# Kernel tuning notes

Hardware: AMD Instinct MI355X
Metric: run time of the kernel (lower is better)

The kernel has to match this reference:

```python
import jax, jax.numpy as jnp
import numpy as np

N, E = 40000, 640000
D, H, DK = 128, 8, 16   # out_dim, n_heads, d_k = D // H
T, R = 3, 4             # num node types, num relation types


def setup_inputs() -> dict:
    key = jax.random.key(0)
    ks = jax.random.split(key, 16)
    glorot = lambda k, shape, fan: jax.random.normal(k, shape, jnp.float32) * np.sqrt(2.0 / fan)
    inp = {
        'node_inp': jax.random.normal(ks[0], (N, D), jnp.float32),
        'node_type': jax.random.randint(ks[1], (N,), 0, T),
        'edge_index': jax.random.randint(ks[2], (2, E), 0, N),
        'edge_type': jax.random.randint(ks[3], (E,), 0, R),
        'node_position': jax.random.randint(ks[4], (N,), 0, N),
        # per-node-type Linear weights, stored [T, in, out] (y = x @ W + b)
        'Kw': glorot(ks[5], (T, D, D), 2 * D), 'Kb': jnp.zeros((T, D), jnp.float32),
        'Qw': glorot(ks[6], (T, D, D), 2 * D), 'Qb': jnp.zeros((T, D), jnp.float32),
        'Vw': glorot(ks[7], (T, D, D), 2 * D), 'Vb': jnp.zeros((T, D), jnp.float32),
        'Aw': glorot(ks[8], (T, D, D), 2 * D), 'Ab': jnp.zeros((T, D), jnp.float32),
        'relation_pri': jnp.ones((T, R, T, H), jnp.float32),
        'relation_att': glorot(ks[9], (R, H, DK, DK), 2 * DK),
        'relation_msg': glorot(ks[10], (R, H, DK, DK), 2 * DK),
        'relation_s2u': glorot(ks[11], (D, D), 2 * D),
        'skip': jnp.ones((T,), jnp.float32),
    }
    return inp


def reference(node_inp, node_type, edge_index, edge_type, node_position,
              Kw, Kb, Qw, Qb, Vw, Vb, Aw, Ab,
              relation_pri, relation_att, relation_msg, relation_s2u, skip):
    n = node_inp.shape[0]
    src, tgt = edge_index[0], edge_index[1]  # j (source), i (target)
    ar = jnp.arange(n)

    # per-type K/Q/V projections for every node: [T, N, D], then select own type
    k_all = jnp.einsum('nd,tdo->tno', node_inp, Kw) + Kb[:, None, :]
    q_all = jnp.einsum('nd,tdo->tno', node_inp, Qw) + Qb[:, None, :]
    v_all = jnp.einsum('nd,tdo->tno', node_inp, Vw) + Vb[:, None, :]
    k_node = k_all[node_type, ar]
    q_node = q_all[node_type, ar]
    v_node = v_all[node_type, ar]

    k_j = k_node[src].reshape(-1, H, DK)
    v_j = v_node[src].reshape(-1, H, DK)
    q_i = q_node[tgt].reshape(-1, H, DK)

    # per-relation attention / message transforms (select per edge relation)
    k_t = jnp.zeros_like(k_j)
    v_t = jnp.zeros_like(v_j)
    for r in range(R):
        sel = (edge_type == r)[:, None, None]
        k_t = jnp.where(sel, jnp.einsum('ehd,hdf->ehf', k_j, relation_att[r]), k_t)
        v_t = jnp.where(sel, jnp.einsum('ehd,hdf->ehf', v_j, relation_msg[r]), v_t)

    st, tt = node_type[src], node_type[tgt]
    pri = relation_pri[tt, edge_type, st]                       # [E, H]
    att_raw = (q_i * k_t).sum(-1) * pri / np.sqrt(DK)           # [E, H]

    # scatter-softmax over edges sharing the same target node
    m = jax.ops.segment_max(att_raw, tgt, num_segments=n)
    m = jnp.where(jnp.isfinite(m), m, 0.0)
    ex = jnp.exp(att_raw - m[tgt])
    den = jax.ops.segment_sum(ex, tgt, num_segments=n)
    att = ex / (den[tgt] + 1e-16)

    msg = (v_t * att[:, :, None]).reshape(-1, D)
    aggr = jax.ops.segment_sum(msg, tgt, num_segments=n)        # scatter-add

    # speaker information: edges with edge_type==0, message from target rep to source index
    sp_in = v_all[1][tgt]                                       # v_linears[1](node_inp[edge_index_i])
    sp_msg = sp_in @ relation_s2u                               # [E, D]
    drop_idx = jnp.where(edge_type == 0, src, n)                # out-of-range -> dropped
    speaker_info = jnp.zeros((n, D), node_inp.dtype).at[drop_idx].set(sp_msg, mode='drop')

    aggr = jax.nn.gelu(aggr + speaker_info, approximate=False)

    # target-specific aggregation with per-type learnable skip (dropout=eval identity)
    a_all = jnp.einsum('no,tof->tnf', aggr, Aw) + Ab[:, None, :]
    a_node = a_all[node_type, ar]
    alpha = jax.nn.sigmoid(skip)[node_type][:, None]
    return a_node * alpha + node_inp * (1.0 - alpha)
```

## Files before the change

kernel.cpp:

```cpp
#include <hip/hip_runtime.h>
#include <hip/hip_bf16.h>
#include <math.h>

#define ND 128
#define NH 8
#define DKK 16
#define NT 3
#define NR 4
#define NB 8
#define NMAT 12
#define SCB 4096

typedef unsigned short ushort_t;
typedef __bf16 bf16_t;
typedef bf16_t bf16x8 __attribute__((ext_vector_type(8)));
typedef float f32x4 __attribute__((ext_vector_type(4)));

__device__ __forceinline__ float bf2f(unsigned short u) {
    union { unsigned int i; float f; } v; v.i = ((unsigned int)u) << 16; return v.f;
}
__device__ __forceinline__ unsigned short f2bf(float f) {
    union { float f; unsigned int i; } v; v.f = f;
    unsigned int x = v.i;
    unsigned int lsb = (x >> 16) & 1u;
    x += 0x7fffu + lsb;
    return (unsigned short)(x >> 16);
}
__device__ __forceinline__ unsigned int pk2(float a, float b) {
    return (unsigned int)f2bf(a) | ((unsigned int)f2bf(b) << 16);
}
__device__ __forceinline__ void load_bf8(const ushort_t* p, float* o) {
    uint4 u = *reinterpret_cast<const uint4*>(p);
    o[0]=bf2f(u.x & 0xffff); o[1]=bf2f(u.x >> 16);
    o[2]=bf2f(u.y & 0xffff); o[3]=bf2f(u.y >> 16);
    o[4]=bf2f(u.z & 0xffff); o[5]=bf2f(u.z >> 16);
    o[6]=bf2f(u.w & 0xffff); o[7]=bf2f(u.w >> 16);
}
__device__ __forceinline__ bf16x8 as_bf16x8(uint4 u) {
    union { uint4 u; bf16x8 v; } c; c.u = u; return c.v;
}


__global__ void k_zero(int n, int* offs, int* winner, int* tcnt) {
    int i = blockIdx.x * 256 + threadIdx.x;
    if (i < n) { offs[i] = 0; winner[i] = -1; }
    if (i < NT) tcnt[i] = 0;
}

__global__ void k_count(int n, int e, const int* src, const int* tgt, const int* etype,
                        const int* ntype, int* offs, int* winner, int* tcnt, int* rank) {
    int i = blockIdx.x * 256 + threadIdx.x;
    if (i < e) {
        rank[i] = atomicAdd(&offs[tgt[i]], 1);
        if (etype[i] == 0) atomicMax(&winner[src[i]], i);
    }
    if (i < n) {
        int t = ntype[i];
        int lane = threadIdx.x & 63;
        #pragma unroll
        for (int tt = 0; tt < NT; tt++) {
            bool me = (t == tt);
            unsigned long long m = __ballot(me);
            if (me) {
                int lower = __popcll(m & ((1ull << lane) - 1ull));
                if (lower == 0) atomicAdd(&tcnt[tt], __popcll(m));
            }
        }
    }
}


__global__ void k_scanA(int n, const int* offs, int* bsum) {
    __shared__ int red[256];
    int b = blockIdx.x, tid = threadIdx.x;
    int base = b * SCB + tid * 16;
    int s = 0;
    #pragma unroll
    for (int i = 0; i < 16; i++) {
        int idx = base + i;
        if (idx < n) s += offs[idx];
    }
    red[tid] = s;
    __syncthreads();
    for (int d = 128; d > 0; d >>= 1) {
        if (tid < d) red[tid] += red[tid + d];
        __syncthreads();
    }
    if (tid == 0) bsum[b] = red[0];
}

__global__ void k_scanB(int nb, const int* bsum, int* boff,
                        const int* tcnt, int* tnext, int* tstart) {
    if (threadIdx.x == 0) {
        int run = 0;
        for (int b = 0; b < nb; b++) { boff[b] = run; run += bsum[b]; }
        int t0 = 0;
        for (int t = 0; t < NT; t++) { tnext[t] = t0; tstart[t] = t0; t0 += tcnt[t]; }
    }
}

__global__ void k_scanC(int n, int* offs, const int* boff) {
    __shared__ int red[256];
    int b = blockIdx.x, tid = threadIdx.x;
    int base = b * SCB + tid * 16;
    int v[16];
    int s = 0;
    #pragma unroll
    for (int i = 0; i < 16; i++) {
        int idx = base + i;
        v[i] = (idx < n) ? offs[idx] : 0;
        s += v[i];
    }
    red[tid] = s;
    __syncthreads();
    for (int d = 1; d < 256; d <<= 1) {
        int vv = (tid >= d) ? red[tid - d] : 0;
        __syncthreads();
        red[tid] += vv;
        __syncthreads();
    }
    int run = boff[b] + red[tid] - s;
    #pragma unroll
    for (int i = 0; i < 16; i++) {
        int idx = base + i;
        if (idx < n) { offs[idx] = run; run += v[i]; }
    }
    if (base <= n && n < base + 16) offs[n] = run;
}

__global__ void k_scatter(int n, int e, const int* src, const int* tgt, const int* etype,
                          const int* ntype, const int* offs, const int* rank,
                          int* eord, int mode, int* tnext, int* order) {
    int i = blockIdx.x * 256 + threadIdx.x;
    if (i < e) {
        int p = offs[tgt[i]] + rank[i];
        if (mode) {
            int s = src[i];
            eord[p] = (s * NR + etype[i]) | (ntype[s] << 28);
        } else {
            eord[p] = i;
        }
    }
    if (i < n) {
        int t = ntype[i];
        int lane = threadIdx.x & 63;
        #pragma unroll
        for (int tt = 0; tt < NT; tt++) {
            bool me = (t == tt);
            unsigned long long m = __ballot(me);
            if (me) {
                int lower = __popcll(m & ((1ull << lane) - 1ull));
                int leader = __ffsll((long long)m) - 1;
                int base = 0;
                if (lane == leader) base = atomicAdd(&tnext[tt], __popcll(m));
                base = __shfl(base, leader, 64);
                order[base + lower] = i;
            }
        }
    }
}


__global__ void k_pack(const float* Qw, const float* Qb, const float* Kw, const float* Kb,
                       const float* Vw, const float* Vb, const float* Aw, const float* Ab,
                       const float* s2u, const float* r_att, const float* r_msg,
                       ushort_t* Wall, float* bcat) {
    int blk = blockIdx.x;
    int kb = blk & 3;
    int c = (blk >> 2) & 7;
    int tm = blk >> 5;
    int m = tm % NMAT, t = tm / NMAT;
    int lane = threadIdx.x;
    int nn = c * 16 + (lane & 15);
    int quad = lane >> 4;
    int k0 = kb * 32 + quad * 8;
    ushort_t* dst = Wall + (size_t)blk * 512 + lane * 8;

    if (m == 0 || m == 5 || m == 10 || m == 11) {
        const float* W; const float* B;
        if (m == 0)       { W = Qw + (size_t)t * ND * ND; B = Qb + t * ND; }
        else if (m == 5)  { W = Vw + (size_t)ND * ND;     B = Vb + ND; }
        else if (m == 10) { W = Aw + (size_t)t * ND * ND; B = Ab + t * ND; }
        else              { W = s2u;                      B = nullptr; }
        #pragma unroll
        for (int j = 0; j < 8; j++) dst[j] = f2bf(W[(size_t)(k0 + j) * ND + nn]);
        if (kb == 0 && quad == 0)
            bcat[(t * NMAT + m) * ND + nn] = B ? B[nn] : 0.f;
    } else {
        int r = (m <= 4) ? (m - 1) : (m - 6);
        const float* W0 = (m <= 4) ? Kw : Vw;
        const float* B0 = (m <= 4) ? Kb : Vb;
        const float* Wr = (m <= 4) ? r_att : r_msg;
        int h = c, f = lane & 15;
        float wcol[16];
        #pragma unroll
        for (int jj = 0; jj < 16; jj++)
            wcol[jj] = Wr[(((size_t)r * NH + h) * DKK + jj) * DKK + f];
        #pragma unroll
        for (int j = 0; j < 8; j++) {
            const float* row = W0 + ((size_t)t * ND + (k0 + j)) * ND + h * DKK;
            float s = 0.f;
            #pragma unroll
            for (int jj = 0; jj < 16; jj++) s += row[jj] * wcol[jj];
            dst[j] = f2bf(s);
        }
        if (kb == 0 && quad == 0) {
            const float* brow = B0 + t * ND + h * DKK;
            float sb = 0.f;
            #pragma unroll
            for (int jj = 0; jj < 16; jj++) sb += brow[jj] * wcol[jj];
            bcat[(t * NMAT + m) * ND + nn] = sb;
        }
    }
}

__global__ void __launch_bounds__(256) k_projm(
    int n, const float* x_in, const int* order,
    const int* tcnt, const int* tstart,
    const ushort_t* Wall, const float* bcat,
    int m0, int nm,
    ushort_t* out_qn, ushort_t* out_kt, ushort_t* out_v1, ushort_t* out_vt)
{
    __shared__ __align__(16) ushort_t xs[4096];
    __shared__ int nodes[32];
    int b = blockIdx.x;
    int nb0 = (tcnt[0] + 31) >> 5, nb1 = (tcnt[1] + 31) >> 5, nb2 = (tcnt[2] + 31) >> 5;
    int t, lb;
    if (b < nb0)                  { t = 0; lb = b; }
    else if (b < nb0 + nb1)       { t = 1; lb = b - nb0; }
    else if (b < nb0 + nb1 + nb2) { t = 2; lb = b - nb0 - nb1; }
    else return;
    int segoff = lb * 32;
    int cnt = min(32, tcnt[t] - segoff);
    int segbase = tstart[t] + segoff;
    int tid = threadIdx.x;
    if (tid < 32) nodes[tid] = (tid < cnt) ? order[segbase + tid] : -1;
    __syncthreads();
    {
        int row = tid >> 3;
        int d0 = (tid & 7) * 16;
        int rt = row >> 4, rl = row & 15;
        int kb = d0 >> 5, q0 = (d0 >> 3) & 3;
        uint4 c0, c1;
        if (row < cnt) {
            const float4* xp4 = (const float4*)(x_in + (size_t)nodes[row] * ND + d0);
            float4 a = xp4[0], b2 = xp4[1], c2 = xp4[2], d4 = xp4[3];
            c0.x = pk2(a.x, a.y);   c0.y = pk2(a.z, a.w);
            c0.z = pk2(b2.x, b2.y); c0.w = pk2(b2.z, b2.w);
            c1.x = pk2(c2.x, c2.y); c1.y = pk2(c2.z, c2.w);
            c1.z = pk2(d4.x, d4.y); c1.w = pk2(d4.z, d4.w);
        } else {
            c0.x = c0.y = c0.z = c0.w = 0u;
            c1 = c0;
        }
        *(uint4*)&xs[((rt * 4 + kb) * 64 + q0 * 16 + rl) * 8]       = c0;
        *(uint4*)&xs[((rt * 4 + kb) * 64 + (q0 + 1) * 16 + rl) * 8] = c1;
    }
    __syncthreads();

    int w = tid >> 6, lane = tid & 63;
    int rt = w & 1;
    bf16x8 afr[4];
    #pragma unroll
    for (int kb = 0; kb < 4; kb++)
        afr[kb] = as_bf16x8(*(const uint4*)&xs[((rt * 4 + kb) * 64 + lane) * 8]);
    int nct = nm * 8;
    for (int ct = (w >> 1); ct < nct; ct += 2) {
        int m = m0 + (ct >> 3), c = ct & 7;
        const uint4* bp = (const uint4*)(Wall + ((((size_t)t * NMAT + m) * 8 + c) * 4) * 512);
        f32x4 acc = {0.f, 0.f, 0.f, 0.f};
        #pragma unroll
        for (int kb = 0; kb < 4; kb++) {
            bf16x8 bfr = as_bf16x8(bp[kb * 64 + lane]);
            acc = __builtin_amdgcn_mfma_f32_16x16x32_bf16(afr[kb], bfr, acc, 0, 0, 0);
        }
        int col = c * 16 + (lane & 15);
        float bias = bcat[(t * NMAT + m) * ND + col];
        int rbase = rt * 16 + (lane >> 4) * 4;
        #pragma unroll
        for (int r = 0; r < 4; r++) {
            int grow = rbase + r;
            if (grow >= cnt) continue;
            int node = nodes[grow];
            ushort_t val = f2bf(acc[r] + bias);
            if (m == 0)       out_qn[(size_t)node * ND + col] = val;
            else if (m <= 4)  out_kt[((size_t)node * NR + (m - 1)) * ND + col] = val;
            else if (m == 5)  out_v1[(size_t)node * ND + col] = val;
            else              out_vt[((size_t)node * NR + (m - 6)) * ND + col] = val;
        }
    }
}

__global__ void __launch_bounds__(256) k_projall(
    int n, const float* x_in, const int* order,
    const int* tcnt, const int* tstart,
    const ushort_t* Wall, const float* bcat,
    ushort_t* out_qn, ushort_t* out_kt, ushort_t* out_v1, ushort_t* out_vt)
{
    __shared__ __align__(16) ushort_t xs[4096];
    __shared__ int nodes[32];
    int b = blockIdx.x;
    int nb0 = (tcnt[0] + 31) >> 5, nb1 = (tcnt[1] + 31) >> 5, nb2 = (tcnt[2] + 31) >> 5;
    int t, lb;
    if (b < nb0)                  { t = 0; lb = b; }
    else if (b < nb0 + nb1)       { t = 1; lb = b - nb0; }
    else if (b < nb0 + nb1 + nb2) { t = 2; lb = b - nb0 - nb1; }
    else return;
    int segoff = lb * 32;
    int cnt = min(32, tcnt[t] - segoff);
    int segbase = tstart[t] + segoff;
    int tid = threadIdx.x;
    if (tid < 32) nodes[tid] = (tid < cnt) ? order[segbase + tid] : -1;
    __syncthreads();
    {
        int row = tid >> 3;
        int d0 = (tid & 7) * 16;
        int rt = row >> 4, rl = row & 15;
        int kb = d0 >> 5, q0 = (d0 >> 3) & 3;
        uint4 c0, c1;
        if (row < cnt) {
            const float4* xp4 = (const float4*)(x_in + (size_t)nodes[row] * ND + d0);
            float4 a = xp4[0], b2 = xp4[1], c2 = xp4[2], d4 = xp4[3];
            c0.x = pk2(a.x, a.y);   c0.y = pk2(a.z, a.w);
            c0.z = pk2(b2.x, b2.y); c0.w = pk2(b2.z, b2.w);
            c1.x = pk2(c2.x, c2.y); c1.y = pk2(c2.z, c2.w);
            c1.z = pk2(d4.x, d4.y); c1.w = pk2(d4.z, d4.w);
        } else {
            c0.x = c0.y = c0.z = c0.w = 0u;
            c1 = c0;
        }
        *(uint4*)&xs[((rt * 4 + kb) * 64 + q0 * 16 + rl) * 8]       = c0;
        *(uint4*)&xs[((rt * 4 + kb) * 64 + (q0 + 1) * 16 + rl) * 8] = c1;
    }
    __syncthreads();

    int w = tid >> 6, lane = tid & 63;
    int rt = w & 1;
    bf16x8 afr[4];
    #pragma unroll
    for (int kb = 0; kb < 4; kb++)
        afr[kb] = as_bf16x8(*(const uint4*)&xs[((rt * 4 + kb) * 64 + lane) * 8]);
    for (int ct = (w >> 1); ct < 80; ct += 2) {
        int m = ct >> 3, c = ct & 7;
        const uint4* bp = (const uint4*)(Wall + ((((size_t)t * NMAT + m) * 8 + c) * 4) * 512);
        f32x4 acc = {0.f, 0.f, 0.f, 0.f};
        #pragma unroll
        for (int kb = 0; kb < 4; kb++) {
            bf16x8 bfr = as_bf16x8(bp[kb * 64 + lane]);
            acc = __builtin_amdgcn_mfma_f32_16x16x32_bf16(afr[kb], bfr, acc, 0, 0, 0);
        }
        int col = c * 16 + (lane & 15);
        float bias = bcat[(t * NMAT + m) * ND + col];
        int rbase = rt * 16 + (lane >> 4) * 4;
        #pragma unroll
        for (int r = 0; r < 4; r++) {
            int grow = rbase + r;
            if (grow >= cnt) continue;
            int node = nodes[grow];
            ushort_t val = f2bf(acc[r] + bias);
            if (m == 0)       out_qn[(size_t)node * ND + col] = val;
            else if (m <= 4)  out_kt[((size_t)node * NR + (m - 1)) * ND + col] = val;
            else if (m == 5)  out_v1[(size_t)node * ND + col] = val;
            else              out_vt[((size_t)node * NR + (m - 6)) * ND + col] = val;
        }
    }
}

__global__ void __launch_bounds__(256) k_flash(
    int n, const int* off, const int* srp, const int* ntype,
    const ushort_t* qn, const ushort_t* kt, const ushort_t* vt,
    const float* r_pri, float* aggr)
{
    int wv = threadIdx.x >> 6, lane = threadIdx.x & 63;
    int i = blockIdx.x * 4 + wv;
    if (i >= n) return;
    int h = lane & 7, slot = lane >> 3;
    int hA = lane >> 3;
    int tt = ntype[i];
    float qf[16];
    load_bf8(qn + (size_t)i * ND + h * DKK, qf);
    load_bf8(qn + (size_t)i * ND + h * DKK + 8, qf + 8);
    const float* prib = r_pri + (size_t)(tt * NR * NT) * NH + h;
    int d0 = off[i], d1 = off[i + 1];
    float m = -3.0e38f, den = 0.f;
    float acc0 = 0.f, acc1 = 0.f;
    for (int p0 = d0; p0 < d1; p0 += 8) {
        int p = p0 + slot;
        bool live = (p < d1);
        int sp = live ? srp[p] : 0;
        int sr = sp & 0x0fffffff;
        int st = ((unsigned int)sp) >> 28;
        int r = sr & (NR - 1);
        float kf[16];
        const ushort_t* kp = kt + (size_t)sr * ND + h * DKK;
        load_bf8(kp, kf);
        load_bf8(kp + 8, kf + 8);
        float a = 0.f;
        #pragma unroll
        for (int f = 0; f < 16; f++) a += qf[f] * kf[f];
        float pri = prib[(r * NT + st) * NH];
        float logit = fminf(fmaxf(a * pri * 0.25f, -1.0e4f), 1.0e4f);
        if (!live) logit = -3.0e38f;
        float cm = logit;
        #pragma unroll
        for (int d = 8; d < 64; d <<= 1) cm = fmaxf(cm, __shfl_xor(cm, d, 64));
        float mnew = fmaxf(m, cm);
        float w = live ? expf(logit - mnew) : 0.f;
        float ws = w;
        #pragma unroll
        for (int d = 8; d < 64; d <<= 1) ws += __shfl_xor(ws, d, 64);
        float scale = expf(m - mnew);
        den = den * scale + ws;
        m = mnew;
        float scaleA = __shfl(scale, hA, 64);
        acc0 *= scaleA; acc1 *= scaleA;
        #pragma unroll
        for (int s = 0; s < 8; s++) {
            if (p0 + s < d1) {
                int srcl = s * 8 + hA;
                int srb  = __shfl(sr, srcl, 64);
                float wb = __shfl(w, srcl, 64);
                unsigned int u = *reinterpret_cast<const unsigned int*>(
                    vt + (size_t)srb * ND + lane * 2);
                acc0 += wb * bf2f(u & 0xffff);
                acc1 += wb * bf2f(u >> 16);
            }
        }
    }
    float denA = __shfl(den, hA, 64);
    float inv = 1.f / (denA + 1e-16f);
    float2 o; o.x = acc0 * inv; o.y = acc1 * inv;
    *reinterpret_cast<float2*>(aggr + (size_t)i * ND + lane * 2) = o;
}

__global__ void __launch_bounds__(256) k_sfinal(
    int n, const float* x_in, const int* order, const int* tcnt, const int* tstart,
    const int* winner, const int* tgt, const ushort_t* v1b,
    const ushort_t* Wall, const float* bcat, const float* skip,
    const float* aggr, float* out)
{
    __shared__ __align__(16) float xf[32 * 132];
    __shared__ __align__(16) ushort_t xs[4096];
    __shared__ int nodes[32];
    __shared__ int wsrc[32];
    int b = blockIdx.x;
    int nb0 = (tcnt[0] + 31) >> 5, nb1 = (tcnt[1] + 31) >> 5, nb2 = (tcnt[2] + 31) >> 5;
    int t, lb;
    if (b < nb0)                  { t = 0; lb = b; }
    else if (b < nb0 + nb1)       { t = 1; lb = b - nb0; }
    else if (b < nb0 + nb1 + nb2) { t = 2; lb = b - nb0 - nb1; }
    else return;
    int segoff = lb * 32;
    int cnt = min(32, tcnt[t] - segoff);
    int segbase = tstart[t] + segoff;
    int tid = threadIdx.x;
    if (tid < 32) {
        int nd = (tid < cnt) ? order[segbase + tid] : -1;
        nodes[tid] = nd;
        int wi = (nd >= 0) ? winner[nd] : -1;
        wsrc[tid] = (wi >= 0) ? tgt[wi] : -1;
    }
    __syncthreads();
    {
        int row = tid >> 3;
        int d0 = (tid & 7) * 16;
        int rt = row >> 4, rl = row & 15;
        int kb = d0 >> 5, q0 = (d0 >> 3) & 3;
        uint4 c0, c1;
        int s = (row < cnt) ? wsrc[row] : -1;
        if (s >= 0) {
            const uint4* vp = (const uint4*)(v1b + (size_t)s * ND + d0);
            c0 = vp[0]; c1 = vp[1];
        } else { c0.x = c0.y = c0.z = c0.w = 0u; c1 = c0; }
        *(uint4*)&xs[((rt * 4 + kb) * 64 + q0 * 16 + rl) * 8]       = c0;
        *(uint4*)&xs[((rt * 4 + kb) * 64 + (q0 + 1) * 16 + rl) * 8] = c1;
    }
    __syncthreads();
    int w = tid >> 6, lane = tid & 63;
    int rt = w & 1;
    {
        bf16x8 afr[4];
        #pragma unroll
        for (int kb = 0; kb < 4; kb++)
            afr[kb] = as_bf16x8(*(const uint4*)&xs[((rt * 4 + kb) * 64 + lane) * 8]);
        for (int ct = (w >> 1); ct < 8; ct += 2) {
            const uint4* bp = (const uint4*)(Wall + (((size_t)11 * 8 + ct) * 4) * 512);
            f32x4 acc = {0.f, 0.f, 0.f, 0.f};
            #pragma unroll
            for (int kb = 0; kb < 4; kb++) {
                bf16x8 bfr = as_bf16x8(bp[kb * 64 + lane]);
                acc = __builtin_amdgcn_mfma_f32_16x16x32_bf16(afr[kb], bfr, acc, 0, 0, 0);
            }
            int col = ct * 16 + (lane & 15);
            int rbase = rt * 16 + (lane >> 4) * 4;
            #pragma unroll
            for (int r = 0; r < 4; r++) {
                int grow = rbase + r;
                if (grow >= cnt) continue;
                int node = nodes[grow];
                float g = aggr[(size_t)node * ND + col] + acc[r];
                g = 0.5f * g * (1.f + erff(g * 0.70710678118f));
                xf[grow * 132 + col] = g;
            }
        }
    }
    __syncthreads();
    {
        int row = tid >> 3;
        int d0 = (tid & 7) * 16;
        int rt2 = row >> 4, rl = row & 15;
        int kb = d0 >> 5, q0 = (d0 >> 3) & 3;
        uint4 c0, c1;
        if (row < cnt) {
            const float4* xp4 = (const float4*)(xf + row * 132 + d0);
            float4 a = xp4[0], b2 = xp4[1], c2 = xp4[2], d4 = xp4[3];
            c0.x = pk2(a.x, a.y);   c0.y = pk2(a.z, a.w);
            c0.z = pk2(b2.x, b2.y); c0.w = pk2(b2.z, b2.w);
            c1.x = pk2(c2.x, c2.y); c1.y = pk2(c2.z, c2.w);
            c1.z = pk2(d4.x, d4.y); c1.w = pk2(d4.z, d4.w);
        } else {
            c0.x = c0.y = c0.z = c0.w = 0u;
            c1 = c0;
        }
        *(uint4*)&xs[((rt2 * 4 + kb) * 64 + q0 * 16 + rl) * 8]       = c0;
        *(uint4*)&xs[((rt2 * 4 + kb) * 64 + (q0 + 1) * 16 + rl) * 8] = c1;
    }
    __syncthreads();
    float alpha = 1.f / (1.f + expf(-skip[t]));
    {
        bf16x8 afr[4];
        #pragma unroll
        for (int kb = 0; kb < 4; kb++)
            afr[kb] = as_bf16x8(*(const uint4*)&xs[((rt * 4 + kb) * 64 + lane) * 8]);
        for (int ct = (w >> 1); ct < 8; ct += 2) {
            const uint4* bp = (const uint4*)(Wall + ((((size_t)t * NMAT + 10) * 8 + ct) * 4) * 512);
            f32x4 acc = {0.f, 0.f, 0.f, 0.f};
            #pragma unroll
            for (int kb = 0; kb < 4; kb++) {
                bf16x8 bfr = as_bf16x8(bp[kb * 64 + lane]);
                acc = __builtin_amdgcn_mfma_f32_16x16x32_bf16(afr[kb], bfr, acc, 0, 0, 0);
            }
            int col = ct * 16 + (lane & 15);
            float bias = bcat[(t * NMAT + 10) * ND + col];
            int rbase = rt * 16 + (lane >> 4) * 4;
            #pragma unroll
            for (int r = 0; r < 4; r++) {
                int grow = rbase + r;
                if (grow >= cnt) continue;
                int node = nodes[grow];
                float xin = x_in[(size_t)node * ND + col];
                out[(size_t)node * ND + col] = (acc[r] + bias) * alpha + xin * (1.f - alpha);
            }
        }
    }
}

__global__ void __launch_bounds__(256) k_attmd(
    int n, const int* off, const int* srp, const int* ntype,
    const ushort_t* qn, const ushort_t* kt, const float* r_pri,
    float* atts, ushort_t* mb, float* db)
{
    int wv = threadIdx.x >> 6, lane = threadIdx.x & 63;
    int i = blockIdx.x * 4 + wv;
    if (i >= n) return;
    int h = lane & 7, slot = lane >> 3;
    int tt = ntype[i];
    float qf[16];
    load_bf8(qn + (size_t)i * ND + h * DKK, qf);
    load_bf8(qn + (size_t)i * ND + h * DKK + 8, qf + 8);
    const float* prib = r_pri + (size_t)(tt * NR * NT) * NH + h;
    int d0 = off[i], d1 = off[i + 1];
    float m = -3.0e38f, den = 0.f;
    #pragma unroll 2
    for (int p0 = d0; p0 < d1; p0 += 8) {
        int p = p0 + slot;
        bool live = (p < d1);
        int sp = live ? srp[p] : 0;
        int sr = sp & 0x0fffffff;
        int st = ((unsigned int)sp) >> 28;
        int r = sr & (NR - 1);
        float kf[16];
        const ushort_t* kp = kt + (size_t)sr * ND + h * DKK;
        load_bf8(kp, kf);
        load_bf8(kp + 8, kf + 8);
        float a = 0.f;
        #pragma unroll
        for (int f = 0; f < 16; f++) a += qf[f] * kf[f];
        float pri = prib[(r * NT + st) * NH];
        float logit = fminf(fmaxf(a * pri * 0.25f, -1.0e4f), 1.0e4f);
        if (live) {
            atts[(size_t)p * NH + h] = logit;
            float mnew = fmaxf(m, logit);
            den = den * expf(m - mnew) + expf(logit - mnew);
            m = mnew;
        }
    }
    #pragma unroll
    for (int d = 8; d < 64; d <<= 1) {
        float mo = __shfl_xor(m, d, 64);
        float dn = __shfl_xor(den, d, 64);
        float mnew = fmaxf(m, mo);
        den = den * expf(m - mnew) + dn * expf(mo - mnew);
        m = mnew;
    }
    if (slot == 0) {
        ushort_t mh = (d1 > d0) ? f2bf(m) : (ushort_t)0;
        float dfin = (d1 > d0) ? den * expf(m - bf2f(mh)) : 0.f;
        mb[i * NH + h] = mh;
        db[i * NH + h] = dfin;
    }
}

__global__ void __launch_bounds__(256) k_aggr_fast(
    int n, const int* off, const int* srp, const ushort_t* vt, const float* atts,
    const ushort_t* mb, const float* db, float* aggr)
{
    int wv = threadIdx.x >> 6, lane = threadIdx.x & 63;
    int i = blockIdx.x * 4 + wv;
    if (i >= n) return;
    int h = lane >> 3;
    float mref = bf2f(mb[i * NH + h]);
    float inv = 1.f / (db[i * NH + h] + 1e-16f);
    int d0 = off[i], d1 = off[i + 1];
    float acc0 = 0.f, acc1 = 0.f;
    #pragma unroll 4
    for (int p = d0; p < d1; p++) {
        int sr = srp[p] & 0x0fffffff;
        float w = expf(atts[(size_t)p * NH + h] - mref) * inv;
        unsigned int u = *reinterpret_cast<const unsigned int*>(
            vt + (size_t)sr * ND + lane * 2);
        acc0 += w * bf2f(u & 0xffff);
        acc1 += w * bf2f(u >> 16);
    }
    float2 o; o.x = acc0; o.y = acc1;
    *reinterpret_cast<float2*>(aggr + (size_t)i * ND + lane * 2) = o;
}


__global__ void k_proj(int n, const float* x_in, const int* ntype, const int* order,
                       const float* Kw, const float* Kb,
                       const float* Qw, const float* Qb,
                       const float* Vw, const float* Vb,
                       ushort_t* kn, ushort_t* qn, ushort_t* vn, ushort_t* v1) {
    __shared__ float xs[NB][ND];
    __shared__ int nodes[NB];
    __shared__ int types[NB];
    int tid = threadIdx.x;
    int base = blockIdx.x * NB;
    int cnt = min(NB, n - base);
    if (tid < cnt) { int nd = order[base + tid]; nodes[tid] = nd; types[tid] = ntype[nd]; }
    __syncthreads();
    for (int j = 0; j < cnt; j++) xs[j][tid] = x_in[(size_t)nodes[j] * ND + tid];
    __syncthreads();
    bool uni = (types[0] == types[cnt - 1]);
    for (int m = 0; m < 4; m++) {
        const float *W, *B; ushort_t* out; int forced_t = -1;
        if (m == 0)      { W = Kw; B = Kb; out = kn; }
        else if (m == 1) { W = Qw; B = Qb; out = qn; }
        else if (m == 2) { W = Vw; B = Vb; out = vn; }
        else             { W = Vw; B = Vb; out = v1; forced_t = 1; }
        if (uni || forced_t >= 0) {
            int t = (forced_t >= 0) ? forced_t : types[0];
            float bias = B[t * ND + tid];
            float acc[NB];
            #pragma unroll
            for (int j = 0; j < NB; j++) acc[j] = bias;
            const float* Wp = W + (size_t)t * ND * ND + tid;
            for (int d = 0; d < ND; d++) {
                float w = Wp[(size_t)d * ND];
                #pragma unroll
                for (int j = 0; j < NB; j++) acc[j] += xs[j][d] * w;
            }
            for (int j = 0; j < cnt; j++) out[(size_t)nodes[j] * ND + tid] = f2bf(acc[j]);
        } else {
            for (int j = 0; j < cnt; j++) {
                int t = types[j];
                float acc = B[t * ND + tid];
                const float* Wp = W + (size_t)t * ND * ND + tid;
                for (int d = 0; d < ND; d++) acc += xs[j][d] * Wp[(size_t)d * ND];
                out[(size_t)nodes[j] * ND + tid] = f2bf(acc);
            }
        }
    }
}

__global__ void k_att(int e, const int* src, const int* tgt, const int* etype, const int* ntype,
                      const ushort_t* kn, const ushort_t* qn,
                      const float* r_att, const float* r_pri, float* att) {
    int id = blockIdx.x * 256 + threadIdx.x;
    if (id >= e * NH) return;
    int ee = id >> 3, h = id & 7;
    int s = src[ee], t = tgt[ee], r = etype[ee];
    float kf[16], qf[16];
    load_bf8(kn + (size_t)s * ND + h * DKK, kf);
    load_bf8(kn + (size_t)s * ND + h * DKK + 8, kf + 8);
    load_bf8(qn + (size_t)t * ND + h * DKK, qf);
    load_bf8(qn + (size_t)t * ND + h * DKK + 8, qf + 8);
    const float* W = r_att + (size_t)(r * NH + h) * DKK * DKK;
    float kt[16];
    #pragma unroll
    for (int f = 0; f < 16; f++) kt[f] = 0.f;
    #pragma unroll 4
    for (int d = 0; d < 16; d++) {
        float kd = kf[d];
        #pragma unroll
        for (int f = 0; f < 16; f++) kt[f] += kd * W[d * 16 + f];
    }
    float a = 0.f;
    #pragma unroll
    for (int f = 0; f < 16; f++) a += qf[f] * kt[f];
    int tt = ntype[t], st = ntype[s];
    float pri = r_pri[((tt * NR + r) * NT + st) * NH + h];
    float logit = a * pri * 0.25f;
    logit = fminf(fmaxf(logit, -1.0e4f), 1.0e4f);
    att[(size_t)ee * NH + h] = logit;
}

__global__ void k_mden(int n, const int* off, const int* sorted,
                       const float* att, ushort_t* mb, float* db) {
    int id = blockIdx.x * 256 + threadIdx.x;
    if (id >= n * NH) return;
    int i = id >> 3, h = id & 7;
    int d0 = off[i], d1 = off[i + 1];
    float m = -3.0e38f;
    for (int p = d0; p < d1; p++) m = fmaxf(m, att[(size_t)sorted[p] * NH + h]);
    ushort_t mh = (d1 > d0) ? f2bf(m) : (ushort_t)0;
    float mref = bf2f(mh);
    float den = 0.f;
    for (int p = d0; p < d1; p++) den += expf(att[(size_t)sorted[p] * NH + h] - mref);
    mb[id] = mh;
    db[id] = den;
}

__global__ void k_norm(int e, const int* tgt, const ushort_t* mb, const float* db, float* att) {
    int id = blockIdx.x * 256 + threadIdx.x;
    if (id >= e * NH) return;
    int ee = id >> 3, h = id & 7;
    int t = tgt[ee];
    float w = expf(att[id] - bf2f(mb[t * NH + h])) / (db[t * NH + h] + 1e-16f);
    att[id] = w;
}

__global__ void k_aggr(int n, const int* off, const int* sorted, const int* src, const int* etype,
                       const ushort_t* vn, const float* r_msg, const float* att, float* aggr) {
    int wv = threadIdx.x >> 6, lane = threadIdx.x & 63;
    int i = blockIdx.x * 4 + wv;
    if (i >= n) return;
    int h = lane >> 3, f0 = (lane & 7) * 2;
    int d0 = off[i], d1 = off[i + 1];
    float acc0 = 0.f, acc1 = 0.f;
    for (int p = d0; p < d1; p++) {
        int ee = sorted[p];
        int s = src[ee], r = etype[ee];
        float w = att[(size_t)ee * NH + h];
        float vj[16];
        load_bf8(vn + (size_t)s * ND + h * DKK, vj);
        load_bf8(vn + (size_t)s * ND + h * DKK + 8, vj + 8);
        const float* Wm = r_msg + (size_t)(r * NH + h) * DKK * DKK + f0;
        float a0 = 0.f, a1 = 0.f;
        #pragma unroll
        for (int d = 0; d < 16; d++) {
            a0 += vj[d] * Wm[d * 16];
            a1 += vj[d] * Wm[d * 16 + 1];
        }
        acc0 += w * a0; acc1 += w * a1;
    }
    aggr[(size_t)i * ND + h * DKK + f0]     = acc0;
    aggr[(size_t)i * ND + h * DKK + f0 + 1] = acc1;
}

__global__ void k_spk(int n, const int* winner, const int* tgt, const ushort_t* v1,
                      const float* s2u, float* aggr) {
    __shared__ float xs[NB][ND];
    __shared__ int wn[NB];
    int tid = threadIdx.x;
    int base = blockIdx.x * NB;
    int cnt = min(NB, n - base);
    if (tid < cnt) wn[tid] = winner[base + tid];
    __syncthreads();
    for (int j = 0; j < cnt; j++) {
        int w = wn[j];
        xs[j][tid] = (w >= 0) ? bf2f(v1[(size_t)tgt[w] * ND + tid]) : 0.f;
    }
    __syncthreads();
    float acc[NB];
    #pragma unroll
    for (int j = 0; j < NB; j++) acc[j] = 0.f;
    const float* Wp = s2u + tid;
    for (int d = 0; d < ND; d++) {
        float w = Wp[(size_t)d * ND];
        #pragma unroll
        for (int j = 0; j < NB; j++) acc[j] += xs[j][d] * w;
    }
    for (int j = 0; j < cnt; j++) {
        size_t idx = (size_t)(base + j) * ND + tid;
        float g = aggr[idx] + acc[j];
        g = 0.5f * g * (1.f + erff(g * 0.70710678118f));
        aggr[idx] = g;
    }
}

__global__ void k_final(int n, const float* x_in, const int* ntype, const int* order,
                        const float* Aw, const float* Ab, const float* skip,
                        const float* aggr, float* out) {
    __shared__ float xs[NB][ND];
    __shared__ int nodes[NB];
    __shared__ int types[NB];
    int tid = threadIdx.x;
    int base = blockIdx.x * NB;
    int cnt = min(NB, n - base);
    if (tid < cnt) { int nd = order[base + tid]; nodes[tid] = nd; types[tid] = ntype[nd]; }
    __syncthreads();
    for (int j = 0; j < cnt; j++) xs[j][tid] = aggr[(size_t)nodes[j] * ND + tid];
    __syncthreads();
    bool uni = (types[0] == types[cnt - 1]);
    if (uni) {
        int t = types[0];
        float bias = Ab[t * ND + tid];
        float acc[NB];
        #pragma unroll
        for (int j = 0; j < NB; j++) acc[j] = bias;
        const float* Wp = Aw + (size_t)t * ND * ND + tid;
        for (int d = 0; d < ND; d++) {
            float w = Wp[(size_t)d * ND];
            #pragma unroll
            for (int j = 0; j < NB; j++) acc[j] += xs[j][d] * w;
        }
        float alpha = 1.f / (1.f + expf(-skip[t]));
        for (int j = 0; j < cnt; j++) {
            float xin = x_in[(size_t)nodes[j] * ND + tid];
            out[(size_t)nodes[j] * ND + tid] = acc[j] * alpha + xin * (1.f - alpha);
        }
    } else {
        for (int j = 0; j < cnt; j++) {
            int t = types[j];
            float acc = Ab[t * ND + tid];
            const float* Wp = Aw + (size_t)t * ND * ND + tid;
            for (int d = 0; d < ND; d++) acc += xs[j][d] * Wp[(size_t)d * ND];
            float alpha = 1.f / (1.f + expf(-skip[t]));
            float xin = x_in[(size_t)nodes[j] * ND + tid];
            out[(size_t)nodes[j] * ND + tid] = acc * alpha + xin * (1.f - alpha);
        }
    }
}

extern "C" void kernel_launch(void* const* d_in, const int* in_sizes, int n_in,
                              void* d_out, int out_size, void* d_ws, size_t ws_size,
                              hipStream_t stream) {
    const float* node_inp = (const float*)d_in[0];
    const int* node_type  = (const int*)d_in[1];
    const int* edge_index = (const int*)d_in[2];
    const int* edge_type  = (const int*)d_in[3];
    const float* Kw = (const float*)d_in[5];
    const float* Kb = (const float*)d_in[6];
    const float* Qw = (const float*)d_in[7];
    const float* Qb = (const float*)d_in[8];
    const float* Vw = (const float*)d_in[9];
    const float* Vb = (const float*)d_in[10];
    const float* Aw = (const float*)d_in[11];
    const float* Ab = (const float*)d_in[12];
    const float* r_pri = (const float*)d_in[13];
    const float* r_att = (const float*)d_in[14];
    const float* r_msg = (const float*)d_in[15];
    const float* s2u   = (const float*)d_in[16];
    const float* skip  = (const float*)d_in[17];

    int n = in_sizes[1];
    int e = in_sizes[3];
    const int* srcp = edge_index;
    const int* tgtp = edge_index + e;

    char* wsp = (char*)d_ws;
    size_t woff = 0;
    auto alloc = [&](size_t b) { void* p = wsp + woff; woff += (b + 255) & ~(size_t)255; return p; };

    int* offs     = (int*)alloc((size_t)(n + 1) * 4);
    int* winner   = (int*)alloc((size_t)n * 4);
    int* order    = (int*)alloc((size_t)n * 4);
    int* tcnt     = (int*)alloc(16);
    int* tnext    = (int*)alloc(16);
    int* tstart   = (int*)alloc(16);
    int* bsum     = (int*)alloc(4096);
    int* boff     = (int*)alloc(4096);
    int* eord     = (int*)alloc((size_t)e * 4);
    ushort_t* mb  = (ushort_t*)alloc((size_t)n * NH * 2);
    float* db     = (float*)alloc((size_t)n * NH * 4);
    ushort_t* v1b = (ushort_t*)alloc((size_t)n * ND * 2);
    float* att    = (float*)alloc((size_t)e * NH * 4);
    size_t commonEnd = woff;

    int* rank = (int*)att;

    woff = commonEnd;
    ushort_t* WallB = (ushort_t*)alloc((size_t)NT * NMAT * 8 * 4 * 512 * 2);
    float* bcatB    = (float*)alloc((size_t)NT * NMAT * ND * 4);
    char* F         = (char*)alloc((size_t)n * 1536);
    size_t fastEnd = woff;

    woff = commonEnd;
    ushort_t* WallA = (ushort_t*)alloc((size_t)NT * NMAT * 8 * 4 * 512 * 2);
    float* bcatA    = (float*)alloc((size_t)NT * NMAT * ND * 4);
    ushort_t* qnA   = (ushort_t*)alloc((size_t)n * ND * 2);
    ushort_t* ktA   = (ushort_t*)alloc((size_t)n * NR * ND * 2);
    ushort_t* vtA   = (ushort_t*)alloc((size_t)n * NR * ND * 2);
    size_t tierAEnd = woff;
    float* aggrA = (float*)att;

    int gn = (n + 255) / 256;
    int ge = (e + 255) / 256;
    int nbscan = n / SCB + 1;
    int gproj = (n + 31) / 32 + NT;

    int tierA = (ws_size >= tierAEnd) && ((size_t)e * NH >= (size_t)n * ND);
    int fast  = (ws_size >= fastEnd);

    k_zero<<<gn, 256, 0, stream>>>(n, offs, winner, tcnt);
    k_count<<<ge, 256, 0, stream>>>(n, e, srcp, tgtp, edge_type, node_type, offs, winner, tcnt, rank);
    k_scanA<<<nbscan, 256, 0, stream>>>(n, offs, bsum);
    k_scanB<<<1, 64, 0, stream>>>(nbscan, bsum, boff, tcnt, tnext, tstart);
    k_scanC<<<nbscan, 256, 0, stream>>>(n, offs, boff);
    k_scatter<<<ge, 256, 0, stream>>>(n, e, srcp, tgtp, edge_type, node_type, offs, rank,
                                      eord, (tierA || fast) ? 1 : 0, tnext, order);

    if (tierA) {
        k_pack<<<NT * NMAT * 8 * 4, 64, 0, stream>>>(Qw, Qb, Kw, Kb, Vw, Vb, Aw, Ab,
                                                     s2u, r_att, r_msg, WallA, bcatA);
        k_projall<<<gproj, 256, 0, stream>>>(n, node_inp, order, tcnt, tstart, WallA, bcatA,
                                             qnA, ktA, v1b, vtA);
        k_flash<<<(n + 3) / 4, 256, 0, stream>>>(n, offs, eord, node_type,
                                                 qnA, ktA, vtA, r_pri, aggrA);
        k_sfinal<<<gproj, 256, 0, stream>>>(n, node_inp, order, tcnt, tstart,
                                            winner, tgtp, v1b, WallA, bcatA, skip,
                                            aggrA, (float*)d_out);
    } else if (fast) {
        ushort_t* qn  = (ushort_t*)F;
        ushort_t* kt  = (ushort_t*)(F + (size_t)n * 256);
        ushort_t* vt  = (ushort_t*)F;
        float* aggr   = (float*)(F + (size_t)n * 1024);

        k_pack<<<NT * NMAT * 8 * 4, 64, 0, stream>>>(Qw, Qb, Kw, Kb, Vw, Vb, Aw, Ab,
                                                     s2u, r_att, r_msg, WallB, bcatB);
        k_projm<<<gproj, 256, 0, stream>>>(n, node_inp, order, tcnt, tstart, WallB, bcatB,
                                           0, 6, qn, kt, v1b, (ushort_t*)nullptr);
        k_attmd<<<(n + 3) / 4, 256, 0, stream>>>(n, offs, eord, node_type,
                                                 qn, kt, r_pri, att, mb, db);
        k_projm<<<gproj, 256, 0, stream>>>(n, node_inp, order, tcnt, tstart, WallB, bcatB,
                                           6, 4, (ushort_t*)nullptr, (ushort_t*)nullptr,
                                           (ushort_t*)nullptr, vt);
        k_aggr_fast<<<(n + 3) / 4, 256, 0, stream>>>(n, offs, eord, vt, att, mb, db, aggr);
        k_sfinal<<<gproj, 256, 0, stream>>>(n, node_inp, order, tcnt, tstart,
                                            winner, tgtp, v1b, WallB, bcatB, skip,
                                            aggr, (float*)d_out);
    } else {
        woff = commonEnd;
        ushort_t* vn  = (ushort_t*)alloc((size_t)n * ND * 2);
        char* regA    = (char*)alloc((size_t)n * ND * 2 * 2);
        ushort_t* kn  = (ushort_t*)regA;
        ushort_t* qn  = (ushort_t*)(regA + (size_t)n * ND * 2);
        float* aggr   = (float*)regA;

        k_proj<<<(n + NB - 1) / NB, 128, 0, stream>>>(n, node_inp, node_type, order,
                                                      Kw, Kb, Qw, Qb, Vw, Vb, kn, qn, vn, v1b);
        k_att<<<(e * NH + 255) / 256, 256, 0, stream>>>(e, srcp, tgtp, edge_type, node_type,
                                                        kn, qn, r_att, r_pri, att);
        k_mden<<<(n * NH + 255) / 256, 256, 0, stream>>>(n, offs, eord, att, mb, db);
        k_norm<<<(e * NH + 255) / 256, 256, 0, stream>>>(e, tgtp, mb, db, att);
        k_aggr<<<(n + 3) / 4, 256, 0, stream>>>(n, offs, eord, srcp, edge_type, vn, r_msg, att, aggr);
        k_spk<<<(n + NB - 1) / NB, 128, 0, stream>>>(n, winner, tgtp, v1b, s2u, aggr);
        k_final<<<(n + NB - 1) / NB, 128, 0, stream>>>(n, node_inp, node_type, order,
                                                       Aw, Ab, skip, aggr, (float*)d_out);
    }
}
```

Baseline: 350.1 us.

## Fold relation attention into query side and apply message transform after aggregation

Instead of projecting K and V per relation for every source node (N×4 rows each), the relation attention matrix is folded into the query projection (4 per-relation queries per target), and plain K and V are stored once per node. In the flash kernel, values are accumulated into four per-relation buckets and the relation message matrix is applied once per target node after aggregation. This cuts the projection GEMM from 10 to 7 matrix slots and shrinks the per-edge gathered K/V rows from relation-expanded tables to single-row tables. In exchange it adds shared-memory query staging, extra register accumulators with branching per edge, and a per-node 16x16 shuffle-based transform at the end.

```diff
diff --git a/kernel.cpp b/kernel.cpp
--- a/kernel.cpp
+++ b/kernel.cpp
@@ -9,6 +9,7 @@
 #define NR 4
 #define NB 8
 #define NMAT 12
+#define NM2 9
 #define SCB 4096
 
 typedef unsigned short ushort_t;
@@ -210,6 +211,57 @@
             #pragma unroll
             for (int jj = 0; jj < 16; jj++) sb += brow[jj] * wcol[jj];
             bcat[(t * NMAT + m) * ND + nn] = sb;
+        }
+    }
+}
+
+__global__ void k_pack2(const float* Qw, const float* Qb, const float* Kw, const float* Kb,
+                        const float* Vw, const float* Vb, const float* Aw, const float* Ab,
+                        const float* s2u, const float* r_att,
+                        ushort_t* Wall, float* bcat) {
+    int blk = blockIdx.x;
+    int kb = blk & 3;
+    int c = (blk >> 2) & 7;
+    int tm = blk >> 5;
+    int m = tm % NM2, t = tm / NM2;
+    int lane = threadIdx.x;
+    int nn = c * 16 + (lane & 15);
+    int quad = lane >> 4;
+    int k0 = kb * 32 + quad * 8;
+    ushort_t* dst = Wall + (size_t)blk * 512 + lane * 8;
+
+    if (m >= 4) {
+        const float* W; const float* B;
+        if (m == 4)      { W = Kw + (size_t)t * ND * ND; B = Kb + t * ND; }
+        else if (m == 5) { W = Vw + (size_t)t * ND * ND; B = Vb + t * ND; }
+        else if (m == 6) { W = Vw + (size_t)ND * ND;     B = Vb + ND; }
+        else if (m == 7) { W = Aw + (size_t)t * ND * ND; B = Ab + t * ND; }
+        else             { W = s2u;                      B = nullptr; }
+        #pragma unroll
+        for (int j = 0; j < 8; j++) dst[j] = f2bf(W[(size_t)(k0 + j) * ND + nn]);
+        if (kb == 0 && quad == 0)
+            bcat[(t * NM2 + m) * ND + nn] = B ? B[nn] : 0.f;
+    } else {
+        int r = m;
+        int h = c, f = lane & 15;
+        float wrow[16];
+        #pragma unroll
+        for (int jj = 0; jj < 16; jj++)
+            wrow[jj] = r_att[(((size_t)r * NH + h) * DKK + f) * DKK + jj];
+        #pragma unroll
+        for (int j = 0; j < 8; j++) {
+            const float* row = Qw + ((size_t)t * ND + (k0 + j)) * ND + h * DKK;
+            float s = 0.f;
+            #pragma unroll
+            for (int jj = 0; jj < 16; jj++) s += row[jj] * wrow[jj];
+            dst[j] = f2bf(s);
+        }
+        if (kb == 0 && quad == 0) {
+            const float* brow = Qb + t * ND + h * DKK;
+            float sb = 0.f;
+            #pragma unroll
+            for (int jj = 0; jj < 16; jj++) sb += brow[jj] * wrow[jj];
+            bcat[(t * NM2 + m) * ND + nn] = sb;
         }
     }
 }
@@ -291,11 +343,11 @@
     }
 }
 
-__global__ void __launch_bounds__(256) k_projall(
+__global__ void __launch_bounds__(256) k_projall2(
     int n, const float* x_in, const int* order,
     const int* tcnt, const int* tstart,
     const ushort_t* Wall, const float* bcat,
-    ushort_t* out_qn, ushort_t* out_kt, ushort_t* out_v1, ushort_t* out_vt)
+    ushort_t* out_qr, ushort_t* out_kn, ushort_t* out_vn, ushort_t* out_v1)
 {
     __shared__ __align__(16) ushort_t xs[4096];
     __shared__ int nodes[32];
@@ -340,9 +392,9 @@
     #pragma unroll
     for (int kb = 0; kb < 4; kb++)
         afr[kb] = as_bf16x8(*(const uint4*)&xs[((rt * 4 + kb) * 64 + lane) * 8]);
-    for (int ct = (w >> 1); ct < 80; ct += 2) {
+    for (int ct = (w >> 1); ct < 56; ct += 2) {
         int m = ct >> 3, c = ct & 7;
-        const uint4* bp = (const uint4*)(Wall + ((((size_t)t * NMAT + m) * 8 + c) * 4) * 512);
+        const uint4* bp = (const uint4*)(Wall + ((((size_t)t * NM2 + m) * 8 + c) * 4) * 512);
         f32x4 acc = {0.f, 0.f, 0.f, 0.f};
         #pragma unroll
         for (int kb = 0; kb < 4; kb++) {
@@ -350,7 +402,7 @@
             acc = __builtin_amdgcn_mfma_f32_16x16x32_bf16(afr[kb], bfr, acc, 0, 0, 0);
         }
         int col = c * 16 + (lane & 15);
-        float bias = bcat[(t * NMAT + m) * ND + col];
+        float bias = bcat[(t * NM2 + m) * ND + col];
         int rbase = rt * 16 + (lane >> 4) * 4;
         #pragma unroll
         for (int r = 0; r < 4; r++) {
@@ -358,32 +410,37 @@
             if (grow >= cnt) continue;
             int node = nodes[grow];
             ushort_t val = f2bf(acc[r] + bias);
-            if (m == 0)       out_qn[(size_t)node * ND + col] = val;
-            else if (m <= 4)  out_kt[((size_t)node * NR + (m - 1)) * ND + col] = val;
-            else if (m == 5)  out_v1[(size_t)node * ND + col] = val;
-            else              out_vt[((size_t)node * NR + (m - 6)) * ND + col] = val;
+            if (m <= 3)       out_qr[((size_t)node * NR + m) * ND + col] = val;
+            else if (m == 4)  out_kn[(size_t)node * ND + col] = val;
+            else if (m == 5)  out_vn[(size_t)node * ND + col] = val;
+            else              out_v1[(size_t)node * ND + col] = val;
         }
     }
 }
 
 __global__ void __launch_bounds__(256) k_flash(
     int n, const int* off, const int* srp, const int* ntype,
-    const ushort_t* qn, const ushort_t* kt, const ushort_t* vt,
-    const float* r_pri, float* aggr)
+    const ushort_t* qr, const ushort_t* kn, const ushort_t* vn,
+    const float* r_pri, const float* r_msg, float* aggr)
 {
+    __shared__ float qs[4][4][132];
     int wv = threadIdx.x >> 6, lane = threadIdx.x & 63;
     int i = blockIdx.x * 4 + wv;
     if (i >= n) return;
-    int h = lane & 7, slot = lane >> 3;
-    int hA = lane >> 3;
+    {
+        int r = lane >> 4, e8 = (lane & 15) * 8;
+        float qv[8];
+        load_bf8(qr + ((size_t)i * NR + r) * ND + e8, qv);
+        #pragma unroll
+        for (int j = 0; j < 8; j++) qs[wv][r][e8 + j] = qv[j];
+    }
+    int h = lane & 7, slot = lane >> 3, hA = lane >> 3;
     int tt = ntype[i];
-    float qf[16];
-    load_bf8(qn + (size_t)i * ND + h * DKK, qf);
-    load_bf8(qn + (size_t)i * ND + h * DKK + 8, qf + 8);
     const float* prib = r_pri + (size_t)(tt * NR * NT) * NH + h;
     int d0 = off[i], d1 = off[i + 1];
     float m = -3.0e38f, den = 0.f;
-    float acc0 = 0.f, acc1 = 0.f;
+    float a00=0.f,a01=0.f,a02=0.f,a03=0.f;
+    float a10=0.f,a11=0.f,a12=0.f,a13=0.f;
     for (int p0 = d0; p0 < d1; p0 += 8) {
         int p = p0 + slot;
         bool live = (p < d1);
@@ -392,9 +449,10 @@
         int st = ((unsigned int)sp) >> 28;
         int r = sr & (NR - 1);
         float kf[16];
-        const ushort_t* kp = kt + (size_t)sr * ND + h * DKK;
+        const ushort_t* kp = kn + (size_t)(sr >> 2) * ND + h * DKK;
         load_bf8(kp, kf);
         load_bf8(kp + 8, kf + 8);
+        const float* qf = &qs[wv][r][h * DKK];
         float a = 0.f;
         #pragma unroll
         for (int f = 0; f < 16; f++) a += qf[f] * kf[f];
@@ -413,23 +471,44 @@
         den = den * scale + ws;
         m = mnew;
         float scaleA = __shfl(scale, hA, 64);
-        acc0 *= scaleA; acc1 *= scaleA;
+        a00*=scaleA; a01*=scaleA; a02*=scaleA; a03*=scaleA;
+        a10*=scaleA; a11*=scaleA; a12*=scaleA; a13*=scaleA;
         #pragma unroll
         for (int s = 0; s < 8; s++) {
             if (p0 + s < d1) {
                 int srcl = s * 8 + hA;
                 int srb  = __shfl(sr, srcl, 64);
                 float wb = __shfl(w, srcl, 64);
+                int rb = srb & 3;
                 unsigned int u = *reinterpret_cast<const unsigned int*>(
-                    vt + (size_t)srb * ND + lane * 2);
-                acc0 += wb * bf2f(u & 0xffff);
-                acc1 += wb * bf2f(u >> 16);
+                    vn + (size_t)(srb >> 2) * ND + lane * 2);
+                float v0 = wb * bf2f(u & 0xffff);
+                float v1 = wb * bf2f(u >> 16);
+                if (rb == 0)      { a00 += v0; a10 += v1; }
+                else if (rb == 1) { a01 += v0; a11 += v1; }
+                else if (rb == 2) { a02 += v0; a12 += v1; }
+                else              { a03 += v0; a13 += v1; }
             }
         }
     }
     float denA = __shfl(den, hA, 64);
     float inv = 1.f / (denA + 1e-16f);
-    float2 o; o.x = acc0 * inv; o.y = acc1 * inv;
+    int f0 = (lane & 7) * 2;
+    float o0 = 0.f, o1 = 0.f;
+    #pragma unroll
+    for (int r = 0; r < 4; r++) {
+        float ar0 = (r == 0) ? a00 : (r == 1) ? a01 : (r == 2) ? a02 : a03;
+        float ar1 = (r == 0) ? a10 : (r == 1) ? a11 : (r == 2) ? a12 : a13;
+        const float* Wm = r_msg + ((size_t)(r * NH + hA) * DKK) * DKK + f0;
+        #pragma unroll
+        for (int d = 0; d < 16; d++) {
+            int srcl = hA * 8 + (d >> 1);
+            float sd = __shfl((d & 1) ? ar1 : ar0, srcl, 64);
+            o0 += sd * Wm[d * DKK];
+            o1 += sd * Wm[d * DKK + 1];
+        }
+    }
+    float2 o; o.x = o0 * inv; o.y = o1 * inv;
     *reinterpret_cast<float2*>(aggr + (size_t)i * ND + lane * 2) = o;
 }
 
@@ -437,7 +516,7 @@
     int n, const float* x_in, const int* order, const int* tcnt, const int* tstart,
     const int* winner, const int* tgt, const ushort_t* v1b,
     const ushort_t* Wall, const float* bcat, const float* skip,
-    const float* aggr, float* out)
+    const float* aggr, float* out, int nmatX, int mA, int mS)
 {
     __shared__ __align__(16) float xf[32 * 132];
     __shared__ __align__(16) ushort_t xs[4096];
@@ -484,7 +563,7 @@
         for (int kb = 0; kb < 4; kb++)
             afr[kb] = as_bf16x8(*(const uint4*)&xs[((rt * 4 + kb) * 64 + lane) * 8]);
         for (int ct = (w >> 1); ct < 8; ct += 2) {
-            const uint4* bp = (const uint4*)(Wall + (((size_t)11 * 8 + ct) * 4) * 512);
+            const uint4* bp = (const uint4*)(Wall + ((((size_t)mS) * 8 + ct) * 4) * 512);
             f32x4 acc = {0.f, 0.f, 0.f, 0.f};
             #pragma unroll
             for (int kb = 0; kb < 4; kb++) {
@@ -533,7 +612,7 @@
         for (int kb = 0; kb < 4; kb++)
             afr[kb] = as_bf16x8(*(const uint4*)&xs[((rt * 4 + kb) * 64 + lane) * 8]);
         for (int ct = (w >> 1); ct < 8; ct += 2) {
-            const uint4* bp = (const uint4*)(Wall + ((((size_t)t * NMAT + 10) * 8 + ct) * 4) * 512);
+            const uint4* bp = (const uint4*)(Wall + ((((size_t)t * nmatX + mA) * 8 + ct) * 4) * 512);
             f32x4 acc = {0.f, 0.f, 0.f, 0.f};
             #pragma unroll
             for (int kb = 0; kb < 4; kb++) {
@@ -541,7 +620,7 @@
                 acc = __builtin_amdgcn_mfma_f32_16x16x32_bf16(afr[kb], bfr, acc, 0, 0, 0);
             }
             int col = ct * 16 + (lane & 15);
-            float bias = bcat[(t * NMAT + 10) * ND + col];
+            float bias = bcat[(t * nmatX + mA) * ND + col];
             int rbase = rt * 16 + (lane >> 4) * 4;
             #pragma unroll
             for (int r = 0; r < 4; r++) {
@@ -898,11 +977,11 @@
     size_t fastEnd = woff;
 
     woff = commonEnd;
-    ushort_t* WallA = (ushort_t*)alloc((size_t)NT * NMAT * 8 * 4 * 512 * 2);
-    float* bcatA    = (float*)alloc((size_t)NT * NMAT * ND * 4);
-    ushort_t* qnA   = (ushort_t*)alloc((size_t)n * ND * 2);
-    ushort_t* ktA   = (ushort_t*)alloc((size_t)n * NR * ND * 2);
-    ushort_t* vtA   = (ushort_t*)alloc((size_t)n * NR * ND * 2);
+    ushort_t* WallA = (ushort_t*)alloc((size_t)NT * NM2 * 8 * 4 * 512 * 2);
+    float* bcatA    = (float*)alloc((size_t)NT * NM2 * ND * 4);
+    ushort_t* qrA   = (ushort_t*)alloc((size_t)n * NR * ND * 2);
+    ushort_t* knA   = (ushort_t*)alloc((size_t)n * ND * 2);
+    ushort_t* vnA   = (ushort_t*)alloc((size_t)n * ND * 2);
     size_t tierAEnd = woff;
     float* aggrA = (float*)att;
 
@@ -923,15 +1002,15 @@
                                       eord, (tierA || fast) ? 1 : 0, tnext, order);
 
     if (tierA) {
-        k_pack<<<NT * NMAT * 8 * 4, 64, 0, stream>>>(Qw, Qb, Kw, Kb, Vw, Vb, Aw, Ab,
-                                                     s2u, r_att, r_msg, WallA, bcatA);
-        k_projall<<<gproj, 256, 0, stream>>>(n, node_inp, order, tcnt, tstart, WallA, bcatA,
-                                             qnA, ktA, v1b, vtA);
+        k_pack2<<<NT * NM2 * 8 * 4, 64, 0, stream>>>(Qw, Qb, Kw, Kb, Vw, Vb, Aw, Ab,
+                                                     s2u, r_att, WallA, bcatA);
+        k_projall2<<<gproj, 256, 0, stream>>>(n, node_inp, order, tcnt, tstart, WallA, bcatA,
+                                              qrA, knA, vnA, v1b);
         k_flash<<<(n + 3) / 4, 256, 0, stream>>>(n, offs, eord, node_type,
-                                                 qnA, ktA, vtA, r_pri, aggrA);
+                                                 qrA, knA, vnA, r_pri, r_msg, aggrA);
         k_sfinal<<<gproj, 256, 0, stream>>>(n, node_inp, order, tcnt, tstart,
                                             winner, tgtp, v1b, WallA, bcatA, skip,
-                                            aggrA, (float*)d_out);
+                                            aggrA, (float*)d_out, NM2, 7, 8);
     } else if (fast) {
         ushort_t* qn  = (ushort_t*)F;
         ushort_t* kt  = (ushort_t*)(F + (size_t)n * 256);
@@ -950,7 +1029,7 @@
         k_aggr_fast<<<(n + 3) / 4, 256, 0, stream>>>(n, offs, eord, vt, att, mb, db, aggr);
         k_sfinal<<<gproj, 256, 0, stream>>>(n, node_inp, order, tcnt, tstart,
                                             winner, tgtp, v1b, WallB, bcatB, skip,
-                                            aggr, (float*)d_out);
+                                            aggr, (float*)d_out, NMAT, 10, 11);
     } else {
         woff = commonEnd;
         ushort_t* vn  = (ushort_t*)alloc((size_t)n * ND * 2);
```

New measurement: 382.7 us. 9.3% more time.
